# Performance work log

Hardware: AMD Instinct MI355X
Metric: run time of the kernel (lower is better)

## Reference

```python
import jax, jax.numpy as jnp
import numpy as np

B, S, H, NH, FF = 16, 1024, 768, 12, 3072
D = H // NH  # 64
EPS = 1e-12


def layer_norm(x, g, b):
    mu = jnp.mean(x, axis=-1, keepdims=True)
    var = jnp.mean(jnp.square(x - mu), axis=-1, keepdims=True)
    return (x - mu) * jax.lax.rsqrt(var + EPS) * g + b


def setup_inputs() -> dict:
    key = jax.random.key(0)
    ks = jax.random.split(key, 16)
    w = lambda k, shape: (jax.random.normal(k, shape, jnp.float32) * 0.02)
    return {
        "features": jax.random.normal(ks[0], (B, S, H), jnp.float32),
        "attention_mask": jnp.zeros((B, S), jnp.float32),  # additive mask
        "wq": w(ks[1], (H, H)), "bq": jnp.zeros((H,), jnp.float32),
        "wk": w(ks[2], (H, H)), "bk": jnp.zeros((H,), jnp.float32),
        "wv": w(ks[3], (H, H)), "bv": jnp.zeros((H,), jnp.float32),
        "wo": w(ks[4], (H, H)), "bo": jnp.zeros((H,), jnp.float32),
        "ln1_g": jnp.ones((H,), jnp.float32), "ln1_b": jnp.zeros((H,), jnp.float32),
        "w1": w(ks[5], (H, FF)), "b1": jnp.zeros((FF,), jnp.float32),
        "w2": w(ks[6], (FF, H)), "b2": jnp.zeros((H,), jnp.float32),
        "ln2_g": jnp.ones((H,), jnp.float32), "ln2_b": jnp.zeros((H,), jnp.float32),
        "wp": w(ks[7], (H, H)), "bp": jnp.zeros((H,), jnp.float32),
        "wm": w(ks[8], (H, 1)), "bm": jnp.zeros((1,), jnp.float32),
    }


def reference(features, attention_mask, wq, bq, wk, bk, wv, bv, wo, bo,
              ln1_g, ln1_b, w1, b1, w2, b2, ln2_g, ln2_b, wp, bp, wm, bm):
    mask = attention_mask[:, None, None, :]  # [B,1,1,S]

    def split_heads(x):  # [B,S,H] -> [B,NH,S,D]
        return x.reshape(B, S, NH, D).transpose(0, 2, 1, 3)

    q = split_heads(features @ wq + bq)
    k = split_heads(features @ wk + bk)
    v = split_heads(features @ wv + bv)

    scores = jnp.einsum("bhqd,bhkd->bhqk", q, k) / np.sqrt(D).astype(np.float32)
    probs = jax.nn.softmax(scores + mask, axis=-1)  # dropout is identity (eval)
    ctx = jnp.einsum("bhqk,bhkd->bhqd", probs, v)
    ctx = ctx.transpose(0, 2, 1, 3).reshape(B, S, H)

    attn_out = layer_norm(ctx @ wo + bo + features, ln1_g, ln1_b)
    ffn = jax.nn.gelu(attn_out @ w1 + b1, approximate=False) @ w2 + b2
    hidden = layer_norm(ffn + attn_out, ln2_g, ln2_b)

    pooled = jnp.tanh(hidden[:, 0] @ wp + bp)  # BertPooler on [CLS]
    cls = (pooled @ wm + bm).squeeze()  # [B]
    return cls
```

## Files before the change

kernel.cpp:

```cpp
#include <hip/hip_runtime.h>
#include <math.h>

namespace {

constexpr int B  = 16;
constexpr int S  = 1024;
constexpr int H  = 768;
constexpr int NH = 12;
constexpr int DH = 64;
constexpr int FF = 3072;
constexpr float EPS = 1e-12f;

__device__ __forceinline__ float waveReduceSum(float v) {
#pragma unroll
    for (int d = 1; d < 64; d <<= 1) v += __shfl_xor(v, d);
    return v;
}

__device__ __forceinline__ float blockReduceSum768(float v, float* red) {
    const int lane = threadIdx.x & 63;
    const int wid  = threadIdx.x >> 6;
    v = waveReduceSum(v);
    __syncthreads();
    if (lane == 0) red[wid] = v;
    __syncthreads();
    float s = 0.f;
#pragma unroll
    for (int w = 0; w < 12; ++w) s += red[w];
    return s;
}

template <int K, int ISPL, int N>
__global__ __launch_bounds__(256) void gemm_partial(
        const float* __restrict__ A, int lda,
        const float* __restrict__ W, float* __restrict__ part) {
    constexpr int IR = K / ISPL;
    __shared__ float Asl[B * IR];
    const int jt  = blockIdx.x;
    const int sp  = blockIdx.y;
    const int i0  = sp * IR;
    const int tid = threadIdx.x;

    for (int e = tid; e < B * IR; e += 256) {
        const int b = e / IR, ii = e % IR;
        Asl[e] = A[(size_t)b * lda + i0 + ii];
    }
    __syncthreads();

    const int jl = tid & 63;
    const int bg = tid >> 6;
    const int j  = jt * 64 + jl;
    const float* wp_ = W + (size_t)i0 * N + j;
    float acc0 = 0.f, acc1 = 0.f, acc2 = 0.f, acc3 = 0.f;
#pragma unroll
    for (int ii = 0; ii < IR; ++ii) {
        const float w = wp_[(size_t)ii * N];
        acc0 += w * Asl[(bg * 4 + 0) * IR + ii];
        acc1 += w * Asl[(bg * 4 + 1) * IR + ii];
        acc2 += w * Asl[(bg * 4 + 2) * IR + ii];
        acc3 += w * Asl[(bg * 4 + 3) * IR + ii];
    }
    float* pp = part + ((size_t)sp * B) * N + j;
    pp[(size_t)(bg * 4 + 0) * N] = acc0;
    pp[(size_t)(bg * 4 + 1) * N] = acc1;
    pp[(size_t)(bg * 4 + 2) * N] = acc2;
    pp[(size_t)(bg * 4 + 3) * N] = acc3;
}

template <int K, int ISPL, int N, int RED>
__global__ __launch_bounds__(256) void gemm_partial_red(
        const float* __restrict__ Ain, const float* __restrict__ bias,
        const float* __restrict__ W, float* __restrict__ part) {
    constexpr int IR = K / ISPL;
    __shared__ float Asl[B * IR];
    const int jt  = blockIdx.x;
    const int sp  = blockIdx.y;
    const int i0  = sp * IR;
    const int tid = threadIdx.x;

    for (int e = tid; e < B * IR; e += 256) {
        const int b = e / IR, ii = e % IR;
        float v = bias[i0 + ii];
#pragma unroll
        for (int sp2 = 0; sp2 < RED; ++sp2)
            v += Ain[((size_t)sp2 * B + b) * K + i0 + ii];
        Asl[e] = v;
    }
    __syncthreads();

    const int jl = tid & 63;
    const int bg = tid >> 6;
    const int j  = jt * 64 + jl;
    const float* wp_ = W + (size_t)i0 * N + j;
    float acc0 = 0.f, acc1 = 0.f, acc2 = 0.f, acc3 = 0.f;
#pragma unroll
    for (int ii = 0; ii < IR; ++ii) {
        const float w = wp_[(size_t)ii * N];
        acc0 += w * Asl[(bg * 4 + 0) * IR + ii];
        acc1 += w * Asl[(bg * 4 + 1) * IR + ii];
        acc2 += w * Asl[(bg * 4 + 2) * IR + ii];
        acc3 += w * Asl[(bg * 4 + 3) * IR + ii];
    }
    float* pp = part + ((size_t)sp * B) * N + j;
    pp[(size_t)(bg * 4 + 0) * N] = acc0;
    pp[(size_t)(bg * 4 + 1) * N] = acc1;
    pp[(size_t)(bg * 4 + 2) * N] = acc2;
    pp[(size_t)(bg * 4 + 3) * N] = acc3;
}

template <int K, int ISPL, int N, int RED>
__global__ __launch_bounds__(256) void gemm_partial_red_gelu(
        const float* __restrict__ Ain, const float* __restrict__ bias,
        const float* __restrict__ W, float* __restrict__ part) {
    constexpr int IR = K / ISPL;
    __shared__ float Asl[B * IR];
    const int jt  = blockIdx.x;
    const int sp  = blockIdx.y;
    const int i0  = sp * IR;
    const int tid = threadIdx.x;

    for (int e = tid; e < B * IR; e += 256) {
        const int b = e / IR, ii = e % IR;
        float v = bias[i0 + ii];
#pragma unroll
        for (int sp2 = 0; sp2 < RED; ++sp2)
            v += Ain[((size_t)sp2 * B + b) * K + i0 + ii];
        Asl[e] = 0.5f * v * (1.0f + erff(v * 0.70710678118654752440f));
    }
    __syncthreads();

    const int jl = tid & 63;
    const int bg = tid >> 6;
    const int j  = jt * 64 + jl;
    const float* wp_ = W + (size_t)i0 * N + j;
    float acc0 = 0.f, acc1 = 0.f, acc2 = 0.f, acc3 = 0.f;
#pragma unroll 32
    for (int ii = 0; ii < IR; ++ii) {
        const float w = wp_[(size_t)ii * N];
        acc0 += w * Asl[(bg * 4 + 0) * IR + ii];
        acc1 += w * Asl[(bg * 4 + 1) * IR + ii];
        acc2 += w * Asl[(bg * 4 + 2) * IR + ii];
        acc3 += w * Asl[(bg * 4 + 3) * IR + ii];
    }
    float* pp = part + ((size_t)sp * B) * N + j;
    pp[(size_t)(bg * 4 + 0) * N] = acc0;
    pp[(size_t)(bg * 4 + 1) * N] = acc1;
    pp[(size_t)(bg * 4 + 2) * N] = acc2;
    pp[(size_t)(bg * 4 + 3) * N] = acc3;
}

__global__ __launch_bounds__(256) void u_kernel(
        const float* __restrict__ q0_part, const float* __restrict__ bq,
        const float* __restrict__ wk, const float* __restrict__ bk,
        float* __restrict__ u, float* __restrict__ constk) {
    const int b = blockIdx.x / NH, h = blockIdx.x % NH;
    __shared__ __align__(16) float qh[DH];
    const int tid = threadIdx.x;
    if (tid < DH) {
        float v = bq[h * DH + tid];
#pragma unroll
        for (int sp = 0; sp < 24; ++sp)
            v += q0_part[((size_t)sp * B + b) * H + h * DH + tid];
        qh[tid] = v;
    }
    __syncthreads();
    if (tid < DH) {
        float v = bk[h * DH + tid] * qh[tid];
        v = waveReduceSum(v);
        if (tid == 0) constk[b * NH + h] = v;
    }
    const int jj = tid & 3, iq = tid >> 2;
    const float4* qv = (const float4*)qh;
    float4 q4[4];
#pragma unroll
    for (int c = 0; c < 4; ++c) q4[c] = qv[jj * 4 + c];
#pragma unroll 4
    for (int ir = 0; ir < 12; ++ir) {
        const int i = ir * 64 + iq;
        const float4* wr = (const float4*)(wk + (size_t)i * H + h * DH);
        float s = 0.f;
#pragma unroll
        for (int c = 0; c < 4; ++c) {
            const float4 w = wr[jj * 4 + c];
            s += w.x * q4[c].x + w.y * q4[c].y + w.z * q4[c].z + w.w * q4[c].w;
        }
        s += __shfl_xor(s, 1);
        s += __shfl_xor(s, 2);
        if (jj == 0) u[((size_t)(b * NH + h)) * H + i] = s;
    }
}

__global__ __launch_bounds__(256, 2) void score_xbar(
        const float* __restrict__ x, const float* __restrict__ u,
        const float* __restrict__ constk, const float* __restrict__ mask,
        float* __restrict__ psum, float* __restrict__ xpart) {
    const int b  = blockIdx.x;
    const int kt = blockIdx.y;
    __shared__ __align__(16) float ul[NH * H];
    __shared__ float e_sh[32 * NH];
    __shared__ float ck[NH];
    __shared__ float wsum[4][NH];
    const int tid = threadIdx.x;
    {
        const float4* ug = (const float4*)(u + (size_t)b * NH * H);
        float4* ul4 = (float4*)ul;
        for (int e = tid; e < NH * H / 4; e += 256) ul4[e] = ug[e];
        if (tid < NH) ck[tid] = constk[b * NH + tid];
    }
    __syncthreads();
    const int jj = tid & 15, kk = tid >> 4;
    const int k0 = kt * 32 + kk * 2;
    float4 xv0[12], xv1[12];
    {
        const float4* xr0 = (const float4*)(x + ((size_t)b * S + k0) * H);
        const float4* xr1 = (const float4*)(x + ((size_t)b * S + k0 + 1) * H);
#pragma unroll
        for (int t = 0; t < 12; ++t) { xv0[t] = xr0[jj + 16 * t]; xv1[t] = xr1[jj + 16 * t]; }
    }
    const float4* ul4 = (const float4*)ul;
    float acc0[NH], acc1[NH];
#pragma unroll
    for (int h = 0; h < NH; ++h) {
        float a0 = 0.f, a1 = 0.f;
#pragma unroll
        for (int t = 0; t < 12; ++t) {
            const float4 uv = ul4[h * 192 + jj + 16 * t];
            a0 += xv0[t].x * uv.x + xv0[t].y * uv.y + xv0[t].z * uv.z + xv0[t].w * uv.w;
            a1 += xv1[t].x * uv.x + xv1[t].y * uv.y + xv1[t].z * uv.z + xv1[t].w * uv.w;
        }
        acc0[h] = a0; acc1[h] = a1;
    }
#pragma unroll
    for (int h = 0; h < NH; ++h) {
#pragma unroll
        for (int d = 1; d < 16; d <<= 1) {
            acc0[h] += __shfl_xor(acc0[h], d);
            acc1[h] += __shfl_xor(acc1[h], d);
        }
    }
    const float mk0 = mask[b * S + k0];
    const float mk1 = mask[b * S + k0 + 1];
    float e0[NH], e1[NH], ps[NH];
#pragma unroll
    for (int h = 0; h < NH; ++h) {
        e0[h] = expf(acc0[h] * 0.125f + ck[h] + mk0);
        e1[h] = expf(acc1[h] * 0.125f + ck[h] + mk1);
        ps[h] = e0[h] + e1[h];
    }
    if (jj == 0) {
#pragma unroll
        for (int h = 0; h < NH; ++h) {
            e_sh[(kk * 2) * NH + h]     = e0[h];
            e_sh[(kk * 2 + 1) * NH + h] = e1[h];
        }
    }
#pragma unroll
    for (int h = 0; h < NH; ++h) {
        ps[h] += __shfl_xor(ps[h], 16);
        ps[h] += __shfl_xor(ps[h], 32);
    }
    const int wid = tid >> 6;
    if ((tid & 63) == 0) {
#pragma unroll
        for (int h = 0; h < NH; ++h) wsum[wid][h] = ps[h];
    }
    __syncthreads();
    if (tid < NH)
        psum[((size_t)(b * 32 + kt)) * NH + tid] =
            wsum[0][tid] + wsum[1][tid] + wsum[2][tid] + wsum[3][tid];

    float aB0[NH], aB1[NH], aB2[NH];
#pragma unroll
    for (int h = 0; h < NH; ++h) { aB0[h] = 0.f; aB1[h] = 0.f; aB2[h] = 0.f; }
    const float* xr = x + ((size_t)b * S + kt * 32) * H;
#pragma unroll 2
    for (int k = 0; k < 32; ++k) {
        const float x0 = xr[(size_t)k * H + tid];
        const float x1 = xr[(size_t)k * H + tid + 256];
        const float x2 = xr[(size_t)k * H + tid + 512];
#pragma unroll
        for (int h = 0; h < NH; ++h) {
            const float ev = e_sh[k * NH + h];
            aB0[h] += ev * x0; aB1[h] += ev * x1; aB2[h] += ev * x2;
        }
    }
    float* op = xpart + ((size_t)(b * 32 + kt)) * NH * H;
#pragma unroll
    for (int h = 0; h < NH; ++h) {
        op[(size_t)h * H + tid]       = aB0[h];
        op[(size_t)h * H + tid + 256] = aB1[h];
        op[(size_t)h * H + tid + 512] = aB2[h];
    }
}

template <int ISPL>
__global__ __launch_bounds__(256) void gemm_xpart(
        const float* __restrict__ xpart, const float* __restrict__ psum,
        const float* __restrict__ W, float* __restrict__ part) {
    constexpr int IR = H / ISPL;
    __shared__ float Asl[B * IR];
    __shared__ float rinv[B];
    const int jt  = blockIdx.x;
    const int sp  = blockIdx.y;
    const int i0  = sp * IR;
    const int tid = threadIdx.x;

    if (tid < B) {
        float s = 0.f;
#pragma unroll
        for (int kt = 0; kt < 32; ++kt)
            s += psum[((size_t)(tid * 32 + kt)) * NH + jt];
        rinv[tid] = 1.0f / s;
    }
    for (int e = tid; e < B * IR; e += 256) {
        const int b = e / IR, ii = e % IR;
        float v = 0.f;
#pragma unroll
        for (int s2 = 0; s2 < 32; ++s2)
            v += xpart[((size_t)(b * 32 + s2)) * NH * H + (size_t)jt * H + i0 + ii];
        Asl[e] = v;
    }
    __syncthreads();

    const int jl = tid & 63, bg = tid >> 6;
    const int j = jt * 64 + jl;
    const float* wp_ = W + (size_t)i0 * H + j;
    float a0 = 0, a1 = 0, a2 = 0, a3 = 0;
#pragma unroll
    for (int ii = 0; ii < IR; ++ii) {
        const float w = wp_[(size_t)ii * H];
        a0 += w * Asl[(bg * 4 + 0) * IR + ii];
        a1 += w * Asl[(bg * 4 + 1) * IR + ii];
        a2 += w * Asl[(bg * 4 + 2) * IR + ii];
        a3 += w * Asl[(bg * 4 + 3) * IR + ii];
    }
    float* pp = part + ((size_t)sp * B) * H + j;
    pp[(size_t)(bg * 4 + 0) * H] = a0 * rinv[bg * 4 + 0];
    pp[(size_t)(bg * 4 + 1) * H] = a1 * rinv[bg * 4 + 1];
    pp[(size_t)(bg * 4 + 2) * H] = a2 * rinv[bg * 4 + 2];
    pp[(size_t)(bg * 4 + 3) * H] = a3 * rinv[bg * 4 + 3];
}

template <int ISPL>
__global__ __launch_bounds__(768) void ln_kernel(
        const float* __restrict__ part, const float* __restrict__ bias,
        const float* __restrict__ resid, int residStride,
        const float* __restrict__ g, const float* __restrict__ bet,
        float* __restrict__ out) {
    __shared__ float red[12];
    const int b = blockIdx.x, j = threadIdx.x;
    float v = bias[j] + resid[(size_t)b * residStride + j];
#pragma unroll
    for (int sp = 0; sp < ISPL; ++sp) v += part[((size_t)sp * B + b) * H + j];
    const float mu = blockReduceSum768(v, red) * (1.0f / H);
    const float d  = v - mu;
    const float var = blockReduceSum768(d * d, red) * (1.0f / H);
    out[(size_t)b * H + j] = d * rsqrtf(var + EPS) * g[j] + bet[j];
}

template <int ISPL>
__global__ __launch_bounds__(768) void cls_kernel(
        const float* __restrict__ part, const float* __restrict__ bp,
        const float* __restrict__ wm, const float* __restrict__ bm,
        float* __restrict__ out) {
    __shared__ float red[12];
    const int b = blockIdx.x, j = threadIdx.x;
    float v = bp[j];
#pragma unroll
    for (int sp = 0; sp < ISPL; ++sp) v += part[((size_t)sp * B + b) * H + j];
    v = tanhf(v);
    const float s = blockReduceSum768(v * wm[j], red);
    if (j == 0) out[b] = s + bm[0];
}

}

extern "C" void kernel_launch(void* const* d_in, const int* in_sizes, int n_in,
                              void* d_out, int out_size, void* d_ws, size_t ws_size,
                              hipStream_t stream) {
    const float* x    = (const float*)d_in[0];
    const float* mask = (const float*)d_in[1];
    const float* wq   = (const float*)d_in[2];
    const float* bq   = (const float*)d_in[3];
    const float* wk   = (const float*)d_in[4];
    const float* bk   = (const float*)d_in[5];
    const float* wv   = (const float*)d_in[6];
    const float* bv   = (const float*)d_in[7];
    const float* wo   = (const float*)d_in[8];
    const float* bo   = (const float*)d_in[9];
    const float* ln1g = (const float*)d_in[10];
    const float* ln1b = (const float*)d_in[11];
    const float* w1   = (const float*)d_in[12];
    const float* b1   = (const float*)d_in[13];
    const float* w2   = (const float*)d_in[14];
    const float* b2   = (const float*)d_in[15];
    const float* ln2g = (const float*)d_in[16];
    const float* ln2b = (const float*)d_in[17];
    const float* wp   = (const float*)d_in[18];
    const float* bp   = (const float*)d_in[19];
    const float* wm   = (const float*)d_in[20];
    const float* bm   = (const float*)d_in[21];
    float* out = (float*)d_out;

    float* ws = (float*)d_ws;
    size_t o = 0;
    float* u         = ws + o; o += (size_t)B * NH * H;
    float* constk    = ws + o; o += 256;
    float* psum      = ws + o; o += (size_t)B * 32 * NH;
    float* attn_out  = ws + o; o += (size_t)B * H;
    float* hidden    = ws + o; o += (size_t)B * H;
    float* xpart     = ws + o; o += (size_t)32 * B * NH * H;
    float* q0_part   = ws + o; o += (size_t)24 * B * H;
    float* ctx_part  = ws + o; o += (size_t)24 * B * H;
    float* wo_part   = ws + o; o += (size_t)24 * B * H;
    float* ffn1_part = ws + o; o += (size_t)24 * B * FF;
    float* ffn2_part = ws + o; o += (size_t)48 * B * H;
    float* pool_part = ws + o; o += (size_t)24 * B * H;
    (void)ws_size; (void)in_sizes; (void)n_in; (void)out_size;

    gemm_partial<H, 24, H><<<dim3(12, 24), 256, 0, stream>>>(x, S * H, wq, q0_part);

    u_kernel<<<B * NH, 256, 0, stream>>>(q0_part, bq, wk, bk, u, constk);

    score_xbar<<<dim3(B, 32), 256, 0, stream>>>(x, u, constk, mask, psum, xpart);

    gemm_xpart<24><<<dim3(12, 24), 256, 0, stream>>>(xpart, psum, wv, ctx_part);

    gemm_partial_red<H, 24, H, 24><<<dim3(12, 24), 256, 0, stream>>>(ctx_part, bv, wo, wo_part);

    ln_kernel<24><<<B, 768, 0, stream>>>(wo_part, bo, x, S * H, ln1g, ln1b, attn_out);

    gemm_partial<H, 24, FF><<<dim3(48, 24), 256, 0, stream>>>(attn_out, H, w1, ffn1_part);

    gemm_partial_red_gelu<FF, 48, H, 24><<<dim3(12, 48), 256, 0, stream>>>(ffn1_part, b1, w2, ffn2_part);

    ln_kernel<48><<<B, 768, 0, stream>>>(ffn2_part, b2, attn_out, H, ln2g, ln2b, hidden);

    gemm_partial<H, 24, H><<<dim3(12, 24), 256, 0, stream>>>(hidden, H, wp, pool_part);

    cls_kernel<24><<<B, 768, 0, stream>>>(pool_part, bp, wm, bm, out);
}
```

Before: 211.1 us.

## Fuse layernorm and classifier tails into GEMMs via last-block tickets; halve score grid

Each GEMM whose output feeds a layernorm or the classifier now does that tail itself. An atomic ticket counter lets the last 16 blocks wait until every partial is written, and each of them reduces one batch row. This removes three small kernel launches and their launch gaps. The score/xbar kernel now handles two key tiles per block on a grid half as tall, which halves the xpart partials that the next GEMM must reduce. The cost is a spin-wait on a global counter, which assumes all blocks are co-resident or scheduled in order, plus less parallelism in the score stage.

Measured after the change: 316.6 us. 1.5x slower.

```diff
diff --git a/kernel.cpp b/kernel.cpp
--- a/kernel.cpp
+++ b/kernel.cpp
@@ -17,29 +17,43 @@
     return v;
 }
 
-__device__ __forceinline__ float blockReduceSum768(float v, float* red) {
-    const int lane = threadIdx.x & 63;
-    const int wid  = threadIdx.x >> 6;
+__device__ __forceinline__ float blockReduce256(float v, float* red) {
+    const int lane = threadIdx.x & 63, wid = threadIdx.x >> 6;
     v = waveReduceSum(v);
     __syncthreads();
     if (lane == 0) red[wid] = v;
     __syncthreads();
-    float s = 0.f;
-#pragma unroll
-    for (int w = 0; w < 12; ++w) s += red[w];
-    return s;
+    return red[0] + red[1] + red[2] + red[3];
+}
+
+__device__ __forceinline__ int lastBlocksTicket(unsigned* counter, unsigned total) {
+    __shared__ unsigned tick_sh;
+    __threadfence();
+    if (threadIdx.x == 0) tick_sh = atomicAdd(counter, 1u);
+    __syncthreads();
+    const unsigned ticket = tick_sh;
+    if (ticket < total - 16) return -1;
+    if (threadIdx.x == 0) {
+        while (atomicAdd(counter, 0u) < total) __builtin_amdgcn_s_sleep(8);
+    }
+    __syncthreads();
+    __threadfence();
+    return (int)(ticket - (total - 16));
 }
 
 template <int K, int ISPL, int N>
 __global__ __launch_bounds__(256) void gemm_partial(
         const float* __restrict__ A, int lda,
-        const float* __restrict__ W, float* __restrict__ part) {
+        const float* __restrict__ W, float* __restrict__ part,
+        unsigned* __restrict__ counters) {
     constexpr int IR = K / ISPL;
     __shared__ float Asl[B * IR];
     const int jt  = blockIdx.x;
     const int sp  = blockIdx.y;
     const int i0  = sp * IR;
     const int tid = threadIdx.x;
+
+    if (counters && jt == 0 && sp == 0 && tid < 8) counters[tid] = 0;
 
     for (int e = tid; e < B * IR; e += 256) {
         const int b = e / IR, ii = e % IR;
@@ -67,12 +81,16 @@
     pp[(size_t)(bg * 4 + 3) * N] = acc3;
 }
 
-template <int K, int ISPL, int N, int RED>
-__global__ __launch_bounds__(256) void gemm_partial_red(
-        const float* __restrict__ Ain, const float* __restrict__ bias,
-        const float* __restrict__ W, float* __restrict__ part) {
-    constexpr int IR = K / ISPL;
+template <int ISPL, int RED>
+__global__ __launch_bounds__(256) void gemm_wo_ln(
+        const float* __restrict__ Ain, const float* __restrict__ biasA,
+        const float* __restrict__ W, float* __restrict__ part,
+        const float* __restrict__ bo, const float* __restrict__ x,
+        const float* __restrict__ g, const float* __restrict__ bet,
+        float* __restrict__ out, unsigned* __restrict__ counter) {
+    constexpr int IR = H / ISPL;
     __shared__ float Asl[B * IR];
+    __shared__ float red[4];
     const int jt  = blockIdx.x;
     const int sp  = blockIdx.y;
     const int i0  = sp * IR;
@@ -80,10 +98,10 @@
 
     for (int e = tid; e < B * IR; e += 256) {
         const int b = e / IR, ii = e % IR;
-        float v = bias[i0 + ii];
+        float v = biasA[i0 + ii];
 #pragma unroll
         for (int sp2 = 0; sp2 < RED; ++sp2)
-            v += Ain[((size_t)sp2 * B + b) * K + i0 + ii];
+            v += Ain[((size_t)sp2 * B + b) * H + i0 + ii];
         Asl[e] = v;
     }
     __syncthreads();
@@ -91,29 +109,55 @@
     const int jl = tid & 63;
     const int bg = tid >> 6;
     const int j  = jt * 64 + jl;
-    const float* wp_ = W + (size_t)i0 * N + j;
+    const float* wp_ = W + (size_t)i0 * H + j;
     float acc0 = 0.f, acc1 = 0.f, acc2 = 0.f, acc3 = 0.f;
 #pragma unroll
     for (int ii = 0; ii < IR; ++ii) {
-        const float w = wp_[(size_t)ii * N];
+        const float w = wp_[(size_t)ii * H];
         acc0 += w * Asl[(bg * 4 + 0) * IR + ii];
         acc1 += w * Asl[(bg * 4 + 1) * IR + ii];
         acc2 += w * Asl[(bg * 4 + 2) * IR + ii];
         acc3 += w * Asl[(bg * 4 + 3) * IR + ii];
     }
-    float* pp = part + ((size_t)sp * B) * N + j;
-    pp[(size_t)(bg * 4 + 0) * N] = acc0;
-    pp[(size_t)(bg * 4 + 1) * N] = acc1;
-    pp[(size_t)(bg * 4 + 2) * N] = acc2;
-    pp[(size_t)(bg * 4 + 3) * N] = acc3;
-}
-
-template <int K, int ISPL, int N, int RED>
-__global__ __launch_bounds__(256) void gemm_partial_red_gelu(
-        const float* __restrict__ Ain, const float* __restrict__ bias,
-        const float* __restrict__ W, float* __restrict__ part) {
-    constexpr int IR = K / ISPL;
+    float* pp = part + ((size_t)sp * B) * H + j;
+    pp[(size_t)(bg * 4 + 0) * H] = acc0;
+    pp[(size_t)(bg * 4 + 1) * H] = acc1;
+    pp[(size_t)(bg * 4 + 2) * H] = acc2;
+    pp[(size_t)(bg * 4 + 3) * H] = acc3;
+
+    const int b = lastBlocksTicket(counter, gridDim.x * gridDim.y);
+    if (b < 0) return;
+    float v[3];
+#pragma unroll
+    for (int c = 0; c < 3; ++c) {
+        const int jj = tid + 256 * c;
+        float t = bo[jj] + x[(size_t)b * S * H + jj];
+#pragma unroll
+        for (int sp2 = 0; sp2 < ISPL; ++sp2)
+            t += part[((size_t)sp2 * B + b) * H + jj];
+        v[c] = t;
+    }
+    const float mu = blockReduce256(v[0] + v[1] + v[2], red) * (1.0f / H);
+    const float d0 = v[0] - mu, d1 = v[1] - mu, d2 = v[2] - mu;
+    const float var = blockReduce256(d0 * d0 + d1 * d1 + d2 * d2, red) * (1.0f / H);
+    const float rs = rsqrtf(var + EPS);
+#pragma unroll
+    for (int c = 0; c < 3; ++c) {
+        const int jj = tid + 256 * c;
+        out[(size_t)b * H + jj] = (v[c] - mu) * rs * g[jj] + bet[jj];
+    }
+}
+
+template <int ISPL, int RED>
+__global__ __launch_bounds__(256) void gemm_ffn2_ln(
+        const float* __restrict__ Ain, const float* __restrict__ b1,
+        const float* __restrict__ W, float* __restrict__ part,
+        const float* __restrict__ b2, const float* __restrict__ resid,
+        const float* __restrict__ g, const float* __restrict__ bet,
+        float* __restrict__ out, unsigned* __restrict__ counter) {
+    constexpr int IR = FF / ISPL;
     __shared__ float Asl[B * IR];
+    __shared__ float red[4];
     const int jt  = blockIdx.x;
     const int sp  = blockIdx.y;
     const int i0  = sp * IR;
@@ -121,10 +165,10 @@
 
     for (int e = tid; e < B * IR; e += 256) {
         const int b = e / IR, ii = e % IR;
-        float v = bias[i0 + ii];
+        float v = b1[i0 + ii];
 #pragma unroll
         for (int sp2 = 0; sp2 < RED; ++sp2)
-            v += Ain[((size_t)sp2 * B + b) * K + i0 + ii];
+            v += Ain[((size_t)sp2 * B + b) * FF + i0 + ii];
         Asl[e] = 0.5f * v * (1.0f + erff(v * 0.70710678118654752440f));
     }
     __syncthreads();
@@ -132,21 +176,99 @@
     const int jl = tid & 63;
     const int bg = tid >> 6;
     const int j  = jt * 64 + jl;
-    const float* wp_ = W + (size_t)i0 * N + j;
+    const float* wp_ = W + (size_t)i0 * H + j;
     float acc0 = 0.f, acc1 = 0.f, acc2 = 0.f, acc3 = 0.f;
-#pragma unroll 32
+#pragma unroll
     for (int ii = 0; ii < IR; ++ii) {
-        const float w = wp_[(size_t)ii * N];
+        const float w = wp_[(size_t)ii * H];
         acc0 += w * Asl[(bg * 4 + 0) * IR + ii];
         acc1 += w * Asl[(bg * 4 + 1) * IR + ii];
         acc2 += w * Asl[(bg * 4 + 2) * IR + ii];
         acc3 += w * Asl[(bg * 4 + 3) * IR + ii];
     }
-    float* pp = part + ((size_t)sp * B) * N + j;
-    pp[(size_t)(bg * 4 + 0) * N] = acc0;
-    pp[(size_t)(bg * 4 + 1) * N] = acc1;
-    pp[(size_t)(bg * 4 + 2) * N] = acc2;
-    pp[(size_t)(bg * 4 + 3) * N] = acc3;
+    float* pp = part + ((size_t)sp * B) * H + j;
+    pp[(size_t)(bg * 4 + 0) * H] = acc0;
+    pp[(size_t)(bg * 4 + 1) * H] = acc1;
+    pp[(size_t)(bg * 4 + 2) * H] = acc2;
+    pp[(size_t)(bg * 4 + 3) * H] = acc3;
+
+    const int b = lastBlocksTicket(counter, gridDim.x * gridDim.y);
+    if (b < 0) return;
+    float v[3];
+#pragma unroll
+    for (int c = 0; c < 3; ++c) {
+        const int jj = tid + 256 * c;
+        float t = b2[jj] + resid[(size_t)b * H + jj];
+#pragma unroll
+        for (int sp2 = 0; sp2 < ISPL; ++sp2)
+            t += part[((size_t)sp2 * B + b) * H + jj];
+        v[c] = t;
+    }
+    const float mu = blockReduce256(v[0] + v[1] + v[2], red) * (1.0f / H);
+    const float d0 = v[0] - mu, d1 = v[1] - mu, d2 = v[2] - mu;
+    const float var = blockReduce256(d0 * d0 + d1 * d1 + d2 * d2, red) * (1.0f / H);
+    const float rs = rsqrtf(var + EPS);
+#pragma unroll
+    for (int c = 0; c < 3; ++c) {
+        const int jj = tid + 256 * c;
+        out[(size_t)b * H + jj] = (v[c] - mu) * rs * g[jj] + bet[jj];
+    }
+}
+
+template <int ISPL>
+__global__ __launch_bounds__(256) void gemm_pool_cls(
+        const float* __restrict__ A, const float* __restrict__ W,
+        float* __restrict__ part,
+        const float* __restrict__ bp, const float* __restrict__ wm,
+        const float* __restrict__ bm, float* __restrict__ out,
+        unsigned* __restrict__ counter) {
+    constexpr int IR = H / ISPL;
+    __shared__ float Asl[B * IR];
+    __shared__ float red[4];
+    const int jt  = blockIdx.x;
+    const int sp  = blockIdx.y;
+    const int i0  = sp * IR;
+    const int tid = threadIdx.x;
+
+    for (int e = tid; e < B * IR; e += 256) {
+        const int b = e / IR, ii = e % IR;
+        Asl[e] = A[(size_t)b * H + i0 + ii];
+    }
+    __syncthreads();
+
+    const int jl = tid & 63;
+    const int bg = tid >> 6;
+    const int j  = jt * 64 + jl;
+    const float* wp_ = W + (size_t)i0 * H + j;
+    float acc0 = 0.f, acc1 = 0.f, acc2 = 0.f, acc3 = 0.f;
+#pragma unroll
+    for (int ii = 0; ii < IR; ++ii) {
+        const float w = wp_[(size_t)ii * H];
+        acc0 += w * Asl[(bg * 4 + 0) * IR + ii];
+        acc1 += w * Asl[(bg * 4 + 1) * IR + ii];
+        acc2 += w * Asl[(bg * 4 + 2) * IR + ii];
+        acc3 += w * Asl[(bg * 4 + 3) * IR + ii];
+    }
+    float* pp = part + ((size_t)sp * B) * H + j;
+    pp[(size_t)(bg * 4 + 0) * H] = acc0;
+    pp[(size_t)(bg * 4 + 1) * H] = acc1;
+    pp[(size_t)(bg * 4 + 2) * H] = acc2;
+    pp[(size_t)(bg * 4 + 3) * H] = acc3;
+
+    const int b = lastBlocksTicket(counter, gridDim.x * gridDim.y);
+    if (b < 0) return;
+    float s = 0.f;
+#pragma unroll
+    for (int c = 0; c < 3; ++c) {
+        const int jj = tid + 256 * c;
+        float t = bp[jj];
+#pragma unroll
+        for (int sp2 = 0; sp2 < ISPL; ++sp2)
+            t += part[((size_t)sp2 * B + b) * H + jj];
+        s += tanhf(t) * wm[jj];
+    }
+    s = blockReduce256(s, red);
+    if (tid == 0) out[b] = s + bm[0];
 }
 
 __global__ __launch_bounds__(256) void u_kernel(
@@ -194,8 +316,8 @@
         const float* __restrict__ x, const float* __restrict__ u,
         const float* __restrict__ constk, const float* __restrict__ mask,
         float* __restrict__ psum, float* __restrict__ xpart) {
-    const int b  = blockIdx.x;
-    const int kt = blockIdx.y;
+    const int b   = blockIdx.x;
+    const int kt0 = blockIdx.y;
     __shared__ __align__(16) float ul[NH * H];
     __shared__ float e_sh[32 * NH];
     __shared__ float ck[NH];
@@ -207,84 +329,88 @@
         for (int e = tid; e < NH * H / 4; e += 256) ul4[e] = ug[e];
         if (tid < NH) ck[tid] = constk[b * NH + tid];
     }
-    __syncthreads();
+    float aB0[NH], aB1[NH], aB2[NH];
+#pragma unroll
+    for (int h = 0; h < NH; ++h) { aB0[h] = 0.f; aB1[h] = 0.f; aB2[h] = 0.f; }
     const int jj = tid & 15, kk = tid >> 4;
-    const int k0 = kt * 32 + kk * 2;
-    float4 xv0[12], xv1[12];
-    {
-        const float4* xr0 = (const float4*)(x + ((size_t)b * S + k0) * H);
-        const float4* xr1 = (const float4*)(x + ((size_t)b * S + k0 + 1) * H);
-#pragma unroll
-        for (int t = 0; t < 12; ++t) { xv0[t] = xr0[jj + 16 * t]; xv1[t] = xr1[jj + 16 * t]; }
-    }
     const float4* ul4 = (const float4*)ul;
-    float acc0[NH], acc1[NH];
-#pragma unroll
-    for (int h = 0; h < NH; ++h) {
-        float a0 = 0.f, a1 = 0.f;
-#pragma unroll
-        for (int t = 0; t < 12; ++t) {
-            const float4 uv = ul4[h * 192 + jj + 16 * t];
-            a0 += xv0[t].x * uv.x + xv0[t].y * uv.y + xv0[t].z * uv.z + xv0[t].w * uv.w;
-            a1 += xv1[t].x * uv.x + xv1[t].y * uv.y + xv1[t].z * uv.z + xv1[t].w * uv.w;
-        }
-        acc0[h] = a0; acc1[h] = a1;
-    }
-#pragma unroll
-    for (int h = 0; h < NH; ++h) {
-#pragma unroll
-        for (int d = 1; d < 16; d <<= 1) {
-            acc0[h] += __shfl_xor(acc0[h], d);
-            acc1[h] += __shfl_xor(acc1[h], d);
-        }
-    }
-    const float mk0 = mask[b * S + k0];
-    const float mk1 = mask[b * S + k0 + 1];
-    float e0[NH], e1[NH], ps[NH];
-#pragma unroll
-    for (int h = 0; h < NH; ++h) {
-        e0[h] = expf(acc0[h] * 0.125f + ck[h] + mk0);
-        e1[h] = expf(acc1[h] * 0.125f + ck[h] + mk1);
-        ps[h] = e0[h] + e1[h];
-    }
-    if (jj == 0) {
+
+    for (int it = 0; it < 2; ++it) {
+        const int kt = kt0 + it * 16;
+        __syncthreads();
+        const int k0 = kt * 32 + kk * 2;
+        float4 xv0[12], xv1[12];
+        {
+            const float4* xr0 = (const float4*)(x + ((size_t)b * S + k0) * H);
+            const float4* xr1 = (const float4*)(x + ((size_t)b * S + k0 + 1) * H);
+#pragma unroll
+            for (int t = 0; t < 12; ++t) { xv0[t] = xr0[jj + 16 * t]; xv1[t] = xr1[jj + 16 * t]; }
+        }
+        float acc0[NH], acc1[NH];
 #pragma unroll
         for (int h = 0; h < NH; ++h) {
-            e_sh[(kk * 2) * NH + h]     = e0[h];
-            e_sh[(kk * 2 + 1) * NH + h] = e1[h];
-        }
-    }
-#pragma unroll
-    for (int h = 0; h < NH; ++h) {
-        ps[h] += __shfl_xor(ps[h], 16);
-        ps[h] += __shfl_xor(ps[h], 32);
-    }
-    const int wid = tid >> 6;
-    if ((tid & 63) == 0) {
-#pragma unroll
-        for (int h = 0; h < NH; ++h) wsum[wid][h] = ps[h];
-    }
-    __syncthreads();
-    if (tid < NH)
-        psum[((size_t)(b * 32 + kt)) * NH + tid] =
-            wsum[0][tid] + wsum[1][tid] + wsum[2][tid] + wsum[3][tid];
-
-    float aB0[NH], aB1[NH], aB2[NH];
-#pragma unroll
-    for (int h = 0; h < NH; ++h) { aB0[h] = 0.f; aB1[h] = 0.f; aB2[h] = 0.f; }
-    const float* xr = x + ((size_t)b * S + kt * 32) * H;
+            float a0 = 0.f, a1 = 0.f;
+#pragma unroll
+            for (int t = 0; t < 12; ++t) {
+                const float4 uv = ul4[h * 192 + jj + 16 * t];
+                a0 += xv0[t].x * uv.x + xv0[t].y * uv.y + xv0[t].z * uv.z + xv0[t].w * uv.w;
+                a1 += xv1[t].x * uv.x + xv1[t].y * uv.y + xv1[t].z * uv.z + xv1[t].w * uv.w;
+            }
+            acc0[h] = a0; acc1[h] = a1;
+        }
+#pragma unroll
+        for (int h = 0; h < NH; ++h) {
+#pragma unroll
+            for (int d = 1; d < 16; d <<= 1) {
+                acc0[h] += __shfl_xor(acc0[h], d);
+                acc1[h] += __shfl_xor(acc1[h], d);
+            }
+        }
+        const float mk0 = mask[b * S + k0];
+        const float mk1 = mask[b * S + k0 + 1];
+        float e0[NH], e1[NH], ps[NH];
+#pragma unroll
+        for (int h = 0; h < NH; ++h) {
+            e0[h] = expf(acc0[h] * 0.125f + ck[h] + mk0);
+            e1[h] = expf(acc1[h] * 0.125f + ck[h] + mk1);
+            ps[h] = e0[h] + e1[h];
+        }
+        if (jj == 0) {
+#pragma unroll
+            for (int h = 0; h < NH; ++h) {
+                e_sh[(kk * 2) * NH + h]     = e0[h];
+                e_sh[(kk * 2 + 1) * NH + h] = e1[h];
+            }
+        }
+#pragma unroll
+        for (int h = 0; h < NH; ++h) {
+            ps[h] += __shfl_xor(ps[h], 16);
+            ps[h] += __shfl_xor(ps[h], 32);
+        }
+        const int wid = tid >> 6;
+        if ((tid & 63) == 0) {
+#pragma unroll
+            for (int h = 0; h < NH; ++h) wsum[wid][h] = ps[h];
+        }
+        __syncthreads();
+        if (tid < NH)
+            psum[((size_t)(b * 32 + kt)) * NH + tid] =
+                wsum[0][tid] + wsum[1][tid] + wsum[2][tid] + wsum[3][tid];
+
+        const float* xr = x + ((size_t)b * S + kt * 32) * H;
 #pragma unroll 2
-    for (int k = 0; k < 32; ++k) {
-        const float x0 = xr[(size_t)k * H + tid];
-        const float x1 = xr[(size_t)k * H + tid + 256];
-        const float x2 = xr[(size_t)k * H + tid + 512];
-#pragma unroll
-        for (int h = 0; h < NH; ++h) {
-            const float ev = e_sh[k * NH + h];
-            aB0[h] += ev * x0; aB1[h] += ev * x1; aB2[h] += ev * x2;
-        }
-    }
-    float* op = xpart + ((size_t)(b * 32 + kt)) * NH * H;
+        for (int k = 0; k < 32; ++k) {
+            const float x0 = xr[(size_t)k * H + tid];
+            const float x1 = xr[(size_t)k * H + tid + 256];
+            const float x2 = xr[(size_t)k * H + tid + 512];
+#pragma unroll
+            for (int h = 0; h < NH; ++h) {
+                const float ev = e_sh[k * NH + h];
+                aB0[h] += ev * x0; aB1[h] += ev * x1; aB2[h] += ev * x2;
+            }
+        }
+    }
+    float* op = xpart + ((size_t)(b * 16 + kt0)) * NH * H;
 #pragma unroll
     for (int h = 0; h < NH; ++h) {
         op[(size_t)h * H + tid]       = aB0[h];
@@ -316,8 +442,8 @@
         const int b = e / IR, ii = e % IR;
         float v = 0.f;
 #pragma unroll
-        for (int s2 = 0; s2 < 32; ++s2)
-            v += xpart[((size_t)(b * 32 + s2)) * NH * H + (size_t)jt * H + i0 + ii];
+        for (int s2 = 0; s2 < 16; ++s2)
+            v += xpart[((size_t)(b * 16 + s2)) * NH * H + (size_t)jt * H + i0 + ii];
         Asl[e] = v;
     }
     __syncthreads();
@@ -342,35 +468,40 @@
 }
 
 template <int ISPL>
-__global__ __launch_bounds__(768) void ln_kernel(
-        const float* __restrict__ part, const float* __restrict__ bias,
-        const float* __restrict__ resid, int residStride,
-        const float* __restrict__ g, const float* __restrict__ bet,
-        float* __restrict__ out) {
-    __shared__ float red[12];
-    const int b = blockIdx.x, j = threadIdx.x;
-    float v = bias[j] + resid[(size_t)b * residStride + j];
-#pragma unroll
-    for (int sp = 0; sp < ISPL; ++sp) v += part[((size_t)sp * B + b) * H + j];
-    const float mu = blockReduceSum768(v, red) * (1.0f / H);
-    const float d  = v - mu;
-    const float var = blockReduceSum768(d * d, red) * (1.0f / H);
-    out[(size_t)b * H + j] = d * rsqrtf(var + EPS) * g[j] + bet[j];
-}
-
-template <int ISPL>
-__global__ __launch_bounds__(768) void cls_kernel(
-        const float* __restrict__ part, const float* __restrict__ bp,
-        const float* __restrict__ wm, const float* __restrict__ bm,
-        float* __restrict__ out) {
-    __shared__ float red[12];
-    const int b = blockIdx.x, j = threadIdx.x;
-    float v = bp[j];
-#pragma unroll
-    for (int sp = 0; sp < ISPL; ++sp) v += part[((size_t)sp * B + b) * H + j];
-    v = tanhf(v);
-    const float s = blockReduceSum768(v * wm[j], red);
-    if (j == 0) out[b] = s + bm[0];
+__global__ __launch_bounds__(256) void gemm_ffn1(
+        const float* __restrict__ A,
+        const float* __restrict__ W, float* __restrict__ part) {
+    constexpr int IR = H / ISPL;
+    __shared__ float Asl[B * IR];
+    const int jt  = blockIdx.x;
+    const int sp  = blockIdx.y;
+    const int i0  = sp * IR;
+    const int tid = threadIdx.x;
+
+    for (int e = tid; e < B * IR; e += 256) {
+        const int b = e / IR, ii = e % IR;
+        Asl[e] = A[(size_t)b * H + i0 + ii];
+    }
+    __syncthreads();
+
+    const int jl = tid & 63;
+    const int bg = tid >> 6;
+    const int j  = jt * 64 + jl;
+    const float* wp_ = W + (size_t)i0 * FF + j;
+    float acc0 = 0.f, acc1 = 0.f, acc2 = 0.f, acc3 = 0.f;
+#pragma unroll
+    for (int ii = 0; ii < IR; ++ii) {
+        const float w = wp_[(size_t)ii * FF];
+        acc0 += w * Asl[(bg * 4 + 0) * IR + ii];
+        acc1 += w * Asl[(bg * 4 + 1) * IR + ii];
+        acc2 += w * Asl[(bg * 4 + 2) * IR + ii];
+        acc3 += w * Asl[(bg * 4 + 3) * IR + ii];
+    }
+    float* pp = part + ((size_t)sp * B) * FF + j;
+    pp[(size_t)(bg * 4 + 0) * FF] = acc0;
+    pp[(size_t)(bg * 4 + 1) * FF] = acc1;
+    pp[(size_t)(bg * 4 + 2) * FF] = acc2;
+    pp[(size_t)(bg * 4 + 3) * FF] = acc3;
 }
 
 }
@@ -404,12 +535,13 @@
 
     float* ws = (float*)d_ws;
     size_t o = 0;
+    unsigned* counters = (unsigned*)(ws); o += 64;
     float* u         = ws + o; o += (size_t)B * NH * H;
     float* constk    = ws + o; o += 256;
     float* psum      = ws + o; o += (size_t)B * 32 * NH;
     float* attn_out  = ws + o; o += (size_t)B * H;
     float* hidden    = ws + o; o += (size_t)B * H;
-    float* xpart     = ws + o; o += (size_t)32 * B * NH * H;
+    float* xpart     = ws + o; o += (size_t)16 * B * NH * H;
     float* q0_part   = ws + o; o += (size_t)24 * B * H;
     float* ctx_part  = ws + o; o += (size_t)24 * B * H;
     float* wo_part   = ws + o; o += (size_t)24 * B * H;
@@ -418,25 +550,22 @@
     float* pool_part = ws + o; o += (size_t)24 * B * H;
     (void)ws_size; (void)in_sizes; (void)n_in; (void)out_size;
 
-    gemm_partial<H, 24, H><<<dim3(12, 24), 256, 0, stream>>>(x, S * H, wq, q0_part);
+    gemm_partial<H, 24, H><<<dim3(12, 24), 256, 0, stream>>>(x, S * H, wq, q0_part, counters);
 
     u_kernel<<<B * NH, 256, 0, stream>>>(q0_part, bq, wk, bk, u, constk);
 
-    score_xbar<<<dim3(B, 32), 256, 0, stream>>>(x, u, constk, mask, psum, xpart);
+    score_xbar<<<dim3(B, 16), 256, 0, stream>>>(x, u, constk, mask, psum, xpart);
 
     gemm_xpart<24><<<dim3(12, 24), 256, 0, stream>>>(xpart, psum, wv, ctx_part);
 
-    gemm_partial_red<H, 24, H, 24><<<dim3(12, 24), 256, 0, stream>>>(ctx_part, bv, wo, wo_part);
-
-    ln_kernel<24><<<B, 768, 0, stream>>>(wo_part, bo, x, S * H, ln1g, ln1b, attn_out);
-
-    gemm_partial<H, 24, FF><<<dim3(48, 24), 256, 0, stream>>>(attn_out, H, w1, ffn1_part);
-
-    gemm_partial_red_gelu<FF, 48, H, 24><<<dim3(12, 48), 256, 0, stream>>>(ffn1_part, b1, w2, ffn2_part);
-
-    ln_kernel<48><<<B, 768, 0, stream>>>(ffn2_part, b2, attn_out, H, ln2g, ln2b, hidden);
-
-    gemm_partial<H, 24, H><<<dim3(12, 24), 256, 0, stream>>>(hidden, H, wp, pool_part);
-
-    cls_kernel<24><<<B, 768, 0, stream>>>(pool_part, bp, wm, bm, out);
-}
+    gemm_wo_ln<24, 24><<<dim3(12, 24), 256, 0, stream>>>(
+        ctx_part, bv, wo, wo_part, bo, x, ln1g, ln1b, attn_out, counters + 0);
+
+    gemm_ffn1<24><<<dim3(48, 24), 256, 0, stream>>>(attn_out, w1, ffn1_part);
+
+    gemm_ffn2_ln<48, 24><<<dim3(12, 48), 256, 0, stream>>>(
+        ffn1_part, b1, w2, ffn2_part, b2, attn_out, ln2g, ln2b, hidden, counters + 1);
+
+    gemm_pool_cls<24><<<dim3(12, 24), 256, 0, stream>>>(
+        hidden, wp, pool_part, bp, wm, bm, out, counters + 2);
+}
```
